# Performance work log

Measured on AMD Instinct MI355X. Metric: run time of the kernel, lower is better.

## Reference

```python
import jax, jax.numpy as jnp
import numpy as np

N_NODES = 50000
N_EDGES = 1_600_000
Q_MULT = 8          # charges_irreps = 8x0e
NODE_MULT = 64      # node_feat_irreps = 64x0e + 64x1o
RBF = 8             # edge_feats_irreps num_irreps
HID = 64            # FullyConnectedNet hidden width
W_NUMEL = 2 * Q_MULT  # edge_tp weight_numel: two uvu paths (0e->0e, 0e x 1o->1o), u=8


def setup_inputs() -> dict:
    key = jax.random.key(0)
    k = jax.random.split(key, 14)
    f = lambda kk, sh: jax.random.normal(kk, sh, dtype=jnp.float32)
    return {
        "node_feats": f(k[0], (N_NODES, NODE_MULT * 4)),          # 64 scalars + 64 vectors(3)
        "charges_0": f(k[1], (N_NODES, Q_MULT)),                  # unused in forward
        "charges_induced": f(k[2], (N_NODES, Q_MULT)),
        "edge_feats": f(k[3], (N_EDGES, RBF)),
        "edge_attrs": f(k[4], (N_EDGES, 4)),                      # Y0 (1) + Y1 (3)
        "field_feats": f(k[5], (N_NODES, RBF)),                   # unused in forward
        "mlp_w1": f(k[6], (RBF, HID)),
        "mlp_w2": f(k[7], (HID, HID)),
        "mlp_w3": f(k[8], (HID, HID)),
        "mlp_w4": f(k[9], (HID, W_NUMEL)),
        "W0": f(k[10], (Q_MULT, NODE_MULT)),                      # node_tp path 0e x 0e -> 0e
        "W1": f(k[11], (Q_MULT, NODE_MULT)),                      # node_tp path 1o x 1o -> 0e
        "edge_index": jax.random.randint(k[12], (2, N_EDGES), 0, N_NODES, dtype=jnp.int32),
        "batch": jnp.zeros((N_NODES,), dtype=jnp.int32),
    }


def reference(node_feats, charges_0, charges_induced, edge_feats, edge_attrs,
              field_feats, mlp_w1, mlp_w2, mlp_w3, mlp_w4, W0, W1,
              edge_index, batch):
    sender, receiver = edge_index[0], edge_index[1]
    num_nodes = node_feats.shape[0]

    # e3nn FullyConnectedNet: variance-normalized linear layers + silu
    h = edge_feats
    for w in (mlp_w1, mlp_w2, mlp_w3):
        h = jax.nn.silu(h @ (w / np.sqrt(np.float32(w.shape[0]))))
    tp_w = h @ (mlp_w4 / np.sqrt(np.float32(mlp_w4.shape[0])))   # [E, 16]
    w0, w1 = tp_w[:, :Q_MULT], tp_w[:, Q_MULT:]                   # per-edge path weights

    # edge_tp (uvu, external weights): gather sender charges, weighted CG product
    q_s = charges_induced[sender]                                  # [E, 8]
    mid0 = (w0 * q_s) * edge_attrs[:, :1]                          # [E, 8]    0e
    mid1 = (w1 * q_s)[:, :, None] * edge_attrs[:, None, 1:4]       # [E, 8, 3] 1o

    # scatter-sum messages to receiver nodes
    sum0 = jax.ops.segment_sum(mid0, receiver, num_segments=num_nodes)
    sum1 = jax.ops.segment_sum(mid1.reshape(-1, Q_MULT * 3), receiver,
                               num_segments=num_nodes).reshape(-1, Q_MULT, 3)

    # node_tp: FullyConnectedTensorProduct(8x0e+8x1o, 64x0e+64x1o -> 1x0e)
    node0 = node_feats[:, :NODE_MULT]                              # [N, 64]
    node1 = node_feats[:, NODE_MULT:].reshape(-1, NODE_MULT, 3)    # [N, 64, 3]
    c = 1.0 / np.sqrt(np.float32(Q_MULT * NODE_MULT * 2))          # path normalization
    e0 = jnp.einsum('nu,nv,uv->n', sum0, node0, W0)
    e1 = jnp.einsum('nuk,nvk,uv->n', sum1, node1, W1) / np.sqrt(np.float32(3.0))  # w3j(1,1,0)
    return c * (e0 + e1)                                           # [N] per-node energy
```

## Files before the change

kernel.cpp:

```cpp
#include <hip/hip_runtime.h>
#include <hip/hip_bf16.h>

typedef short short8 __attribute__((ext_vector_type(8)));
typedef float f32x4 __attribute__((ext_vector_type(4)));

static __device__ __forceinline__ float bf2f(unsigned int b) { return __uint_as_float(b << 16); }
static __device__ __forceinline__ short fb2s(float x) {
    unsigned u = __float_as_uint(x);
    return (short)((u + 0x7FFFu + ((u >> 16) & 1u)) >> 16);
}
static __device__ __forceinline__ unsigned int pack2(float lo, float hi) {
    unsigned int r;
    asm("v_cvt_pk_bf16_f32 %0, %1, %2" : "=v"(r) : "v"(lo), "v"(hi));
    return r;
}
static __device__ __forceinline__ float hsilu(float y) {
    return y * __builtin_amdgcn_rcpf(1.0f + __builtin_amdgcn_exp2f(-y));
}
static __device__ __forceinline__ float load1(const void* p, long off, int isbf) {
    return isbf ? bf2f(((const unsigned short*)p)[off]) : ((const float*)p)[off];
}
static __device__ __forceinline__ void load4(const void* p, long off, int isbf, float* o) {
    if (isbf) {
        uint2 v = *(const uint2*)((const unsigned short*)p + off);
        o[0]=bf2f(v.x&0xffffu); o[1]=bf2f(v.x>>16);
        o[2]=bf2f(v.y&0xffffu); o[3]=bf2f(v.y>>16);
    } else {
        float4 v = *(const float4*)((const float*)p + off);
        o[0]=v.x; o[1]=v.y; o[2]=v.z; o[3]=v.w;
    }
}
static __device__ __forceinline__ int detect_bf16(const void* nf) {
    const unsigned int* w = (const unsigned int*)nf;
    int lane = threadIdx.x & 63;
    unsigned int e = (w[lane] >> 7) & 0xFFu;
    unsigned long long m = __ballot(e >= 118u && e <= 132u);
    return __popcll(m) >= 32 ? 1 : 0;
}

#define NB 32
__global__ __launch_bounds__(256) void k_node(
    const void* __restrict__ nf, const void* __restrict__ W0, const void* __restrict__ W1,
    const void* __restrict__ w1, const void* __restrict__ w2,
    const void* __restrict__ w3, const void* __restrict__ w4,
    short* __restrict__ Bws, float* __restrict__ NA, float* __restrict__ acc, int n_nodes) {
    __shared__ float Nd0[NB * 68];
    __shared__ float Nd1[3 * NB * 68];
    __shared__ float W0L[8 * 68];
    __shared__ float W1L[8 * 68];
    const int tid = threadIdx.x;
    const int isbf = detect_bf16(nf);
    const long n0 = (long)blockIdx.x * NB;

    if (blockIdx.x < 44) {
        int idx = blockIdx.x * 256 + tid;
        int j = idx & 7, lane = (idx >> 3) & 63, tile = idx >> 9;
        int n16 = lane & 15, kq = lane >> 4;
        float v;
        if (tile < 4) {
            int k = kq * 8 + j, n = tile * 16 + n16;
            v = (k < 8) ? load1(w1, k * 64 + n, isbf) * (0.35355339059327373f * 1.4426950408889634f) : 0.0f;
        } else if (tile < 12) {
            int t = (tile - 4) >> 1, kt = (tile - 4) & 1;
            int k = kt * 32 + kq * 8 + j, n = t * 16 + n16;
            v = load1(w2, k * 64 + n, isbf) * 0.125f;
        } else if (tile < 20) {
            int t = (tile - 12) >> 1, kt = (tile - 12) & 1;
            int k = kt * 32 + kq * 8 + j, n = t * 16 + n16;
            v = load1(w3, k * 64 + n, isbf) * 0.125f;
        } else {
            int kt = tile - 20;
            int k = kt * 32 + kq * 8 + j, n = n16;
            v = load1(w4, k * 16 + n, isbf) * (0.125f * 0.6931471805599453f);
        }
        Bws[idx] = fb2s(v);
    }
    if (tid < NB) {
        long n = n0 + tid;
        if (n < n_nodes) acc[n] = 0.0f;
    }
    if (n0 >= n_nodes) return;

    for (int i = tid; i < 512; i += 256) {
        W0L[(i >> 6) * 68 + (i & 63)] = load1(W0, i, isbf);
        W1L[(i >> 6) * 68 + (i & 63)] = load1(W1, i, isbf);
    }
    if (isbf) {
        for (int i = tid; i < NB * 32; i += 256) {
            int node = i >> 5, c8 = (i & 31) * 8;
            long ng = n0 + node; if (ng > n_nodes - 1) ng = n_nodes - 1;
            uint4 v = *(const uint4*)((const unsigned short*)nf + ng * 256 + c8);
            float f[8];
            f[0]=bf2f(v.x&0xffffu); f[1]=bf2f(v.x>>16);
            f[2]=bf2f(v.y&0xffffu); f[3]=bf2f(v.y>>16);
            f[4]=bf2f(v.z&0xffffu); f[5]=bf2f(v.z>>16);
            f[6]=bf2f(v.w&0xffffu); f[7]=bf2f(v.w>>16);
            #pragma unroll
            for (int t = 0; t < 8; t++) {
                int col = c8 + t;
                if (col < 64) Nd0[node * 68 + col] = f[t];
                else {
                    int cc = col - 64, vv = cc / 3, kk = cc - vv * 3;
                    Nd1[(kk * NB + node) * 68 + vv] = f[t];
                }
            }
        }
    } else {
        for (int i = tid; i < NB * 64; i += 256) {
            int node = i >> 6, c4 = (i & 63) * 4;
            long ng = n0 + node; if (ng > n_nodes - 1) ng = n_nodes - 1;
            float4 v = *(const float4*)((const float*)nf + ng * 256 + c4);
            float f[4] = {v.x, v.y, v.z, v.w};
            #pragma unroll
            for (int t = 0; t < 4; t++) {
                int col = c4 + t;
                if (col < 64) Nd0[node * 68 + col] = f[t];
                else {
                    int cc = col - 64, vv = cc / 3, kk = cc - vv * 3;
                    Nd1[(kk * NB + node) * 68 + vv] = f[t];
                }
            }
        }
    }
    __syncthreads();

    const int wv = tid >> 6, lane = tid & 63;
    const int u = lane & 7, ln = lane >> 3;
    float sum[4] = {0.0f, 0.0f, 0.0f, 0.0f};

    if (wv == 0) {
        const float* w = &W0L[u * 68];
        for (int v0 = 0; v0 < 64; v0 += 4) {
            float4 w4 = *(const float4*)(w + v0);
            #pragma unroll
            for (int j = 0; j < 4; j++) {
                float4 nd = *(const float4*)&Nd0[(ln + 8 * j) * 68 + v0];
                sum[j] += w4.x * nd.x + w4.y * nd.y + w4.z * nd.z + w4.w * nd.w;
            }
        }
        #pragma unroll
        for (int j = 0; j < 4; j++) {
            long node = n0 + ln + 8 * j;
            if (node < n_nodes) NA[node * 32 + u] = sum[j] * 0.03125f;
        }
    } else {
        const int kk = wv - 1;
        const float* w = &W1L[u * 68];
        const float* nd1 = &Nd1[kk * NB * 68];
        for (int v0 = 0; v0 < 64; v0 += 4) {
            float4 w4 = *(const float4*)(w + v0);
            #pragma unroll
            for (int j = 0; j < 4; j++) {
                float4 nd = *(const float4*)&nd1[(ln + 8 * j) * 68 + v0];
                sum[j] += w4.x * nd.x + w4.y * nd.y + w4.z * nd.z + w4.w * nd.w;
            }
        }
        #pragma unroll
        for (int j = 0; j < 4; j++) {
            long node = n0 + ln + 8 * j;
            if (node < n_nodes) NA[node * 32 + 8 + u * 3 + kk] = sum[j] * 0.018042195912175804f;
        }
    }
}

__global__ __launch_bounds__(256, 4) void k_edges_mfma(
    const void* __restrict__ ef, const void* __restrict__ ea, const void* __restrict__ qc,
    const int* __restrict__ eidx, const void* __restrict__ nf,
    const short* __restrict__ Bws, const float* __restrict__ NA,
    float* __restrict__ acc, int n_edges) {
    __shared__ __align__(16) short W[11264];
    __shared__ __align__(16) short Hs[4 * 2304];
    const int tid = threadIdx.x, lane = tid & 63, wv = tid >> 6;
    const int n16 = lane & 15, kq = lane >> 4;
    const int isbf = detect_bf16(nf);

    {
        const uint4* src = (const uint4*)Bws;
        uint4* dst = (uint4*)W;
        for (int i = tid; i < 1408; i += 256) dst[i] = src[i];
    }
    __syncthreads();

    short* Hw = Hs + wv * 2304;
    const int rbit = (n16 >> 3) & 1;
    const int wrow = n16 * 72 + ((kq & 1) << 2);
    const int kql = (kq & 1) << 2;
    const f32x4 zero = {0.0f, 0.0f, 0.0f, 0.0f};

    for (int half = 0; half < 2; half++) {
        const long E0 = (long)blockIdx.x * 256 + half * 128 + wv * 32;

        long e_[2]; long ec_[2]; int s_[2], r_[2]; float eav_[2][4];
        #pragma unroll
        for (int mt = 0; mt < 2; mt++) {
            e_[mt] = E0 + mt * 16 + n16;
            long ec = e_[mt]; if (ec > n_edges - 1) ec = n_edges - 1;
            ec_[mt] = ec;
            s_[mt] = eidx[ec];
            r_[mt] = eidx[(long)n_edges + ec];
            load4(ea, ec * 4, isbf, eav_[mt]);
        }

        short8 a1[2];
        #pragma unroll
        for (int mt = 0; mt < 2; mt++) {
            short8 a = {0,0,0,0,0,0,0,0};
            if (kq == 0) {
                if (isbf) {
                    a = *(const short8*)((const unsigned short*)ef + ec_[mt] * 8);
                } else {
                    const float* pe = (const float*)ef + ec_[mt] * 8;
                    float4 v0 = *(const float4*)pe, v1 = *(const float4*)(pe + 4);
                    a[0]=fb2s(v0.x); a[1]=fb2s(v0.y); a[2]=fb2s(v0.z); a[3]=fb2s(v0.w);
                    a[4]=fb2s(v1.x); a[5]=fb2s(v1.y); a[6]=fb2s(v1.z); a[7]=fb2s(v1.w);
                }
            }
            a1[mt] = a;
        }

        {
            f32x4 c1[2][4];
            #pragma unroll
            for (int t = 0; t < 4; t++) {
                short8 b = *(const short8*)(W + t * 512 + lane * 8);
                #pragma unroll
                for (int mt = 0; mt < 2; mt++)
                    c1[mt][t] = __builtin_amdgcn_mfma_f32_16x16x32_bf16(b, a1[mt], zero, 0, 0, 0);
            }
            #pragma unroll
            for (int mt = 0; mt < 2; mt++)
                #pragma unroll
                for (int t = 0; t < 4; t++) {
                    uint2 pkd;
                    pkd.x = pack2(hsilu(c1[mt][t][0]), hsilu(c1[mt][t][1]));
                    pkd.y = pack2(hsilu(c1[mt][t][2]), hsilu(c1[mt][t][3]));
                    *(uint2*)(Hw + mt * 1152 + wrow + (((t * 2 + (kq >> 1)) ^ rbit) << 3)) = pkd;
                }
        }

        float q4_[2][4], na_[2][12];
        #pragma unroll
        for (int mt = 0; mt < 2; mt++) {
            load4(qc, (long)s_[mt] * 8 + kql, isbf, q4_[mt]);
            const float* nr = NA + (long)r_[mt] * 32;
            if (kq < 2) {
                *(float4*)na_[mt] = *(const float4*)(nr + (kq << 2));
            } else {
                *(float4*)(na_[mt] + 0) = *(const float4*)(nr + 8 + (kq - 2) * 12);
                *(float4*)(na_[mt] + 4) = *(const float4*)(nr + 12 + (kq - 2) * 12);
                *(float4*)(na_[mt] + 8) = *(const float4*)(nr + 16 + (kq - 2) * 12);
            }
        }

        #pragma unroll
        for (int L = 0; L < 2; L++) {
            const int base = (L == 0) ? 4 : 12;
            short8 aH[2][2];
            #pragma unroll
            for (int mt = 0; mt < 2; mt++)
                #pragma unroll
                for (int kt = 0; kt < 2; kt++)
                    aH[mt][kt] = *(const short8*)(Hw + mt * 1152 + n16 * 72 + (((kt * 4 + kq) ^ rbit) << 3));
            f32x4 c2[2][4];
            #pragma unroll
            for (int mt = 0; mt < 2; mt++)
                #pragma unroll
                for (int t = 0; t < 4; t++) c2[mt][t] = zero;
            #pragma unroll
            for (int kt = 0; kt < 2; kt++)
                #pragma unroll
                for (int t = 0; t < 4; t++) {
                    short8 b = *(const short8*)(W + (base + t * 2 + kt) * 512 + lane * 8);
                    #pragma unroll
                    for (int mt = 0; mt < 2; mt++)
                        c2[mt][t] = __builtin_amdgcn_mfma_f32_16x16x32_bf16(b, aH[mt][kt], c2[mt][t], 0, 0, 0);
                }
            #pragma unroll
            for (int mt = 0; mt < 2; mt++)
                #pragma unroll
                for (int t = 0; t < 4; t++) {
                    uint2 pkd;
                    pkd.x = pack2(hsilu(c2[mt][t][0]), hsilu(c2[mt][t][1]));
                    pkd.y = pack2(hsilu(c2[mt][t][2]), hsilu(c2[mt][t][3]));
                    *(uint2*)(Hw + mt * 1152 + wrow + (((t * 2 + (kq >> 1)) ^ rbit) << 3)) = pkd;
                }
        }

        f32x4 c4[2] = {zero, zero};
        {
            short8 aH[2][2];
            #pragma unroll
            for (int mt = 0; mt < 2; mt++)
                #pragma unroll
                for (int kt = 0; kt < 2; kt++)
                    aH[mt][kt] = *(const short8*)(Hw + mt * 1152 + n16 * 72 + (((kt * 4 + kq) ^ rbit) << 3));
            #pragma unroll
            for (int kt = 0; kt < 2; kt++) {
                short8 b = *(const short8*)(W + (20 + kt) * 512 + lane * 8);
                #pragma unroll
                for (int mt = 0; mt < 2; mt++)
                    c4[mt] = __builtin_amdgcn_mfma_f32_16x16x32_bf16(b, aH[mt][kt], c4[mt], 0, 0, 0);
            }
        }

        #pragma unroll
        for (int mt = 0; mt < 2; mt++) {
            float p = 0.0f;
            if (kq < 2) {
                #pragma unroll
                for (int r = 0; r < 4; r++) p += c4[mt][r] * q4_[mt][r] * na_[mt][r];
                p *= eav_[mt][0];
            } else {
                #pragma unroll
                for (int r = 0; r < 4; r++) {
                    float d = eav_[mt][1] * na_[mt][r * 3] + eav_[mt][2] * na_[mt][r * 3 + 1]
                            + eav_[mt][3] * na_[mt][r * 3 + 2];
                    p += c4[mt][r] * q4_[mt][r] * d;
                }
            }
            p += __shfl_xor(p, 16);
            p += __shfl_xor(p, 32);
            if (kq == 0 && e_[mt] < n_edges) atomicAdd(&acc[r_[mt]], p);
        }
    }
}

__global__ void k_out(const float* __restrict__ acc, void* __restrict__ out,
                      const void* __restrict__ nf, int n) {
    const int isbf = detect_bf16(nf);
    int i = blockIdx.x * 256 + threadIdx.x;
    if (i >= n) return;
    if (isbf) ((__hip_bfloat16*)out)[i] = __float2bfloat16(acc[i]);
    else      ((float*)out)[i] = acc[i];
}

extern "C" void kernel_launch(void* const* d_in, const int* in_sizes, int n_in,
                              void* d_out, int out_size, void* d_ws, size_t ws_size,
                              hipStream_t stream) {
    const void* node_feats      = d_in[0];
    const void* charges_induced = d_in[2];
    const void* edge_feats      = d_in[3];
    const void* edge_attrs      = d_in[4];
    const void* mlp_w1          = d_in[6];
    const void* mlp_w2          = d_in[7];
    const void* mlp_w3          = d_in[8];
    const void* mlp_w4          = d_in[9];
    const void* W0              = d_in[10];
    const void* W1              = d_in[11];
    const int*  edge_index      = (const int*)d_in[12];

    const int n_nodes = in_sizes[0] / 256;
    const int n_edges = in_sizes[3] / 8;

    short* Bws = (short*)d_ws;
    float* NA  = (float*)((char*)d_ws + 22528);
    float* acc = NA + (size_t)n_nodes * 32;

    int nblk = (n_nodes + NB - 1) / NB;
    if (nblk < 44) nblk = 44;
    k_node<<<nblk, 256, 0, stream>>>(node_feats, W0, W1,
        mlp_w1, mlp_w2, mlp_w3, mlp_w4, Bws, NA, acc, n_nodes);
    k_edges_mfma<<<(n_edges + 255) / 256, 256, 0, stream>>>(
        edge_feats, edge_attrs, charges_induced, edge_index, node_feats, Bws, NA, acc, n_edges);
    k_out<<<(n_nodes + 255) / 256, 256, 0, stream>>>(acc, d_out, node_feats, n_nodes);
}
```

Baseline: 378.8 us.

## Pass MLP activations between MFMA layers via ds_bpermute instead of LDS staging

Permutes the hidden-layer weight columns (Fmap) so MFMA output fragments can be rearranged into the next layer's A-operand layout in registers with a few ds_bpermute ops, removing the per-wave LDS scratch buffer and its write/read round trips. The gathers of charges and node aggregates are moved to just before their use. This reduces LDS footprint and traffic, which may allow higher occupancy. The risks are correctness of the permutation mapping and higher register pressure. Moving the loads later also gives less latency hiding.

```diff
diff --git a/kernel.cpp b/kernel.cpp
--- a/kernel.cpp
+++ b/kernel.cpp
@@ -3,6 +3,7 @@
 
 typedef short short8 __attribute__((ext_vector_type(8)));
 typedef float f32x4 __attribute__((ext_vector_type(4)));
+typedef unsigned int u32x4 __attribute__((ext_vector_type(4)));
 
 static __device__ __forceinline__ float bf2f(unsigned int b) { return __uint_as_float(b << 16); }
 static __device__ __forceinline__ short fb2s(float x) {
@@ -36,6 +37,14 @@
     unsigned int e = (w[lane] >> 7) & 0xFFu;
     unsigned long long m = __ballot(e >= 118u && e <= 132u);
     return __popcll(m) >= 32 ? 1 : 0;
+}
+static __device__ __forceinline__ short8 u4_to_s8(u32x4 u) {
+    union { u32x4 u; short8 s; } cvt; cvt.u = u; return cvt.s;
+}
+
+static __device__ __forceinline__ int Fmap(int tp, int rr) {
+    int kq_s = rr >> 2, h = (rr >> 1) & 1, b = rr & 1;
+    return 32 * (tp >> 1) + 8 * ((kq_s + tp) & 3) + 2 * (2 * h + (tp & 1)) + b;
 }
 
 #define NB 32
@@ -58,15 +67,15 @@
         int n16 = lane & 15, kq = lane >> 4;
         float v;
         if (tile < 4) {
-            int k = kq * 8 + j, n = tile * 16 + n16;
+            int k = kq * 8 + j, n = Fmap(tile, n16);
             v = (k < 8) ? load1(w1, k * 64 + n, isbf) * (0.35355339059327373f * 1.4426950408889634f) : 0.0f;
         } else if (tile < 12) {
             int t = (tile - 4) >> 1, kt = (tile - 4) & 1;
-            int k = kt * 32 + kq * 8 + j, n = t * 16 + n16;
+            int k = kt * 32 + kq * 8 + j, n = Fmap(t, n16);
             v = load1(w2, k * 64 + n, isbf) * 0.125f;
         } else if (tile < 20) {
             int t = (tile - 12) >> 1, kt = (tile - 12) & 1;
-            int k = kt * 32 + kq * 8 + j, n = t * 16 + n16;
+            int k = kt * 32 + kq * 8 + j, n = Fmap(t, n16);
             v = load1(w3, k * 64 + n, isbf) * 0.125f;
         } else {
             int kt = tile - 20;
@@ -169,7 +178,6 @@
     const short* __restrict__ Bws, const float* __restrict__ NA,
     float* __restrict__ acc, int n_edges) {
     __shared__ __align__(16) short W[11264];
-    __shared__ __align__(16) short Hs[4 * 2304];
     const int tid = threadIdx.x, lane = tid & 63, wv = tid >> 6;
     const int n16 = lane & 15, kq = lane >> 4;
     const int isbf = detect_bf16(nf);
@@ -181,35 +189,29 @@
     }
     __syncthreads();
 
-    short* Hw = Hs + wv * 2304;
-    const int rbit = (n16 >> 3) & 1;
-    const int wrow = n16 * 72 + ((kq & 1) << 2);
+    const int A1 = ((lane - 16) & 63) << 2;
+    const int A2 = ((lane - 32) & 63) << 2;
+    const int A3 = ((lane - 48) & 63) << 2;
     const int kql = (kq & 1) << 2;
     const f32x4 zero = {0.0f, 0.0f, 0.0f, 0.0f};
 
     for (int half = 0; half < 2; half++) {
         const long E0 = (long)blockIdx.x * 256 + half * 128 + wv * 32;
 
-        long e_[2]; long ec_[2]; int s_[2], r_[2]; float eav_[2][4];
+        int s_[2], r_[2]; float eav_[2][4];
+        short8 a1[2];
         #pragma unroll
         for (int mt = 0; mt < 2; mt++) {
-            e_[mt] = E0 + mt * 16 + n16;
-            long ec = e_[mt]; if (ec > n_edges - 1) ec = n_edges - 1;
-            ec_[mt] = ec;
+            long ec = E0 + mt * 16 + n16; if (ec > n_edges - 1) ec = n_edges - 1;
             s_[mt] = eidx[ec];
             r_[mt] = eidx[(long)n_edges + ec];
             load4(ea, ec * 4, isbf, eav_[mt]);
-        }
-
-        short8 a1[2];
-        #pragma unroll
-        for (int mt = 0; mt < 2; mt++) {
             short8 a = {0,0,0,0,0,0,0,0};
             if (kq == 0) {
                 if (isbf) {
-                    a = *(const short8*)((const unsigned short*)ef + ec_[mt] * 8);
+                    a = *(const short8*)((const unsigned short*)ef + ec * 8);
                 } else {
-                    const float* pe = (const float*)ef + ec_[mt] * 8;
+                    const float* pe = (const float*)ef + ec * 8;
                     float4 v0 = *(const float4*)pe, v1 = *(const float4*)(pe + 4);
                     a[0]=fb2s(v0.x); a[1]=fb2s(v0.y); a[2]=fb2s(v0.z); a[3]=fb2s(v0.w);
                     a[4]=fb2s(v1.x); a[5]=fb2s(v1.y); a[6]=fb2s(v1.z); a[7]=fb2s(v1.w);
@@ -218,54 +220,45 @@
             a1[mt] = a;
         }
 
-        {
-            f32x4 c1[2][4];
-            #pragma unroll
-            for (int t = 0; t < 4; t++) {
-                short8 b = *(const short8*)(W + t * 512 + lane * 8);
-                #pragma unroll
-                for (int mt = 0; mt < 2; mt++)
-                    c1[mt][t] = __builtin_amdgcn_mfma_f32_16x16x32_bf16(b, a1[mt], zero, 0, 0, 0);
-            }
+        f32x4 c[2][4];
+        short8 aH[2][2];
+
+        #pragma unroll
+        for (int t = 0; t < 4; t++) {
+            short8 b = *(const short8*)(W + t * 512 + lane * 8);
+            #pragma unroll
+            for (int mt = 0; mt < 2; mt++)
+                c[mt][t] = __builtin_amdgcn_mfma_f32_16x16x32_bf16(b, a1[mt], zero, 0, 0, 0);
+        }
+        #pragma unroll
+        for (int mt = 0; mt < 2; mt++) {
+            unsigned p00 = pack2(hsilu(c[mt][0][0]), hsilu(c[mt][0][1]));
+            unsigned p01 = pack2(hsilu(c[mt][0][2]), hsilu(c[mt][0][3]));
+            unsigned p10 = pack2(hsilu(c[mt][1][0]), hsilu(c[mt][1][1]));
+            unsigned p11 = pack2(hsilu(c[mt][1][2]), hsilu(c[mt][1][3]));
+            unsigned p20 = pack2(hsilu(c[mt][2][0]), hsilu(c[mt][2][1]));
+            unsigned p21 = pack2(hsilu(c[mt][2][2]), hsilu(c[mt][2][3]));
+            unsigned p30 = pack2(hsilu(c[mt][3][0]), hsilu(c[mt][3][1]));
+            unsigned p31 = pack2(hsilu(c[mt][3][2]), hsilu(c[mt][3][3]));
+            unsigned q01 = (unsigned)__builtin_amdgcn_ds_bpermute(A1, (int)p10);
+            unsigned q03 = (unsigned)__builtin_amdgcn_ds_bpermute(A1, (int)p11);
+            unsigned q10 = (unsigned)__builtin_amdgcn_ds_bpermute(A2, (int)p20);
+            unsigned q12 = (unsigned)__builtin_amdgcn_ds_bpermute(A2, (int)p21);
+            unsigned q11 = (unsigned)__builtin_amdgcn_ds_bpermute(A3, (int)p30);
+            unsigned q13 = (unsigned)__builtin_amdgcn_ds_bpermute(A3, (int)p31);
+            u32x4 u0 = {p00, q01, p01, q03};
+            u32x4 u1 = {q10, q11, q12, q13};
+            aH[mt][0] = u4_to_s8(u0);
+            aH[mt][1] = u4_to_s8(u1);
+        }
+
+        #pragma unroll
+        for (int L = 0; L < 2; L++) {
+            const int base = (L == 0) ? 4 : 12;
             #pragma unroll
             for (int mt = 0; mt < 2; mt++)
                 #pragma unroll
-                for (int t = 0; t < 4; t++) {
-                    uint2 pkd;
-                    pkd.x = pack2(hsilu(c1[mt][t][0]), hsilu(c1[mt][t][1]));
-                    pkd.y = pack2(hsilu(c1[mt][t][2]), hsilu(c1[mt][t][3]));
-                    *(uint2*)(Hw + mt * 1152 + wrow + (((t * 2 + (kq >> 1)) ^ rbit) << 3)) = pkd;
-                }
-        }
-
-        float q4_[2][4], na_[2][12];
-        #pragma unroll
-        for (int mt = 0; mt < 2; mt++) {
-            load4(qc, (long)s_[mt] * 8 + kql, isbf, q4_[mt]);
-            const float* nr = NA + (long)r_[mt] * 32;
-            if (kq < 2) {
-                *(float4*)na_[mt] = *(const float4*)(nr + (kq << 2));
-            } else {
-                *(float4*)(na_[mt] + 0) = *(const float4*)(nr + 8 + (kq - 2) * 12);
-                *(float4*)(na_[mt] + 4) = *(const float4*)(nr + 12 + (kq - 2) * 12);
-                *(float4*)(na_[mt] + 8) = *(const float4*)(nr + 16 + (kq - 2) * 12);
-            }
-        }
-
-        #pragma unroll
-        for (int L = 0; L < 2; L++) {
-            const int base = (L == 0) ? 4 : 12;
-            short8 aH[2][2];
-            #pragma unroll
-            for (int mt = 0; mt < 2; mt++)
-                #pragma unroll
-                for (int kt = 0; kt < 2; kt++)
-                    aH[mt][kt] = *(const short8*)(Hw + mt * 1152 + n16 * 72 + (((kt * 4 + kq) ^ rbit) << 3));
-            f32x4 c2[2][4];
-            #pragma unroll
-            for (int mt = 0; mt < 2; mt++)
-                #pragma unroll
-                for (int t = 0; t < 4; t++) c2[mt][t] = zero;
+                for (int t = 0; t < 4; t++) c[mt][t] = zero;
             #pragma unroll
             for (int kt = 0; kt < 2; kt++)
                 #pragma unroll
@@ -273,54 +266,69 @@
                     short8 b = *(const short8*)(W + (base + t * 2 + kt) * 512 + lane * 8);
                     #pragma unroll
                     for (int mt = 0; mt < 2; mt++)
-                        c2[mt][t] = __builtin_amdgcn_mfma_f32_16x16x32_bf16(b, aH[mt][kt], c2[mt][t], 0, 0, 0);
-                }
+                        c[mt][t] = __builtin_amdgcn_mfma_f32_16x16x32_bf16(b, aH[mt][kt], c[mt][t], 0, 0, 0);
+                }
+            #pragma unroll
+            for (int mt = 0; mt < 2; mt++) {
+                unsigned p00 = pack2(hsilu(c[mt][0][0]), hsilu(c[mt][0][1]));
+                unsigned p01 = pack2(hsilu(c[mt][0][2]), hsilu(c[mt][0][3]));
+                unsigned p10 = pack2(hsilu(c[mt][1][0]), hsilu(c[mt][1][1]));
+                unsigned p11 = pack2(hsilu(c[mt][1][2]), hsilu(c[mt][1][3]));
+                unsigned p20 = pack2(hsilu(c[mt][2][0]), hsilu(c[mt][2][1]));
+                unsigned p21 = pack2(hsilu(c[mt][2][2]), hsilu(c[mt][2][3]));
+                unsigned p30 = pack2(hsilu(c[mt][3][0]), hsilu(c[mt][3][1]));
+                unsigned p31 = pack2(hsilu(c[mt][3][2]), hsilu(c[mt][3][3]));
+                unsigned q01 = (unsigned)__builtin_amdgcn_ds_bpermute(A1, (int)p10);
+                unsigned q03 = (unsigned)__builtin_amdgcn_ds_bpermute(A1, (int)p11);
+                unsigned q10 = (unsigned)__builtin_amdgcn_ds_bpermute(A2, (int)p20);
+                unsigned q12 = (unsigned)__builtin_amdgcn_ds_bpermute(A2, (int)p21);
+                unsigned q11 = (unsigned)__builtin_amdgcn_ds_bpermute(A3, (int)p30);
+                unsigned q13 = (unsigned)__builtin_amdgcn_ds_bpermute(A3, (int)p31);
+                u32x4 u0 = {p00, q01, p01, q03};
+                u32x4 u1 = {q10, q11, q12, q13};
+                aH[mt][0] = u4_to_s8(u0);
+                aH[mt][1] = u4_to_s8(u1);
+            }
+        }
+
+        f32x4 c4[2] = {zero, zero};
+        #pragma unroll
+        for (int kt = 0; kt < 2; kt++) {
+            short8 b = *(const short8*)(W + (20 + kt) * 512 + lane * 8);
             #pragma unroll
             for (int mt = 0; mt < 2; mt++)
-                #pragma unroll
-                for (int t = 0; t < 4; t++) {
-                    uint2 pkd;
-                    pkd.x = pack2(hsilu(c2[mt][t][0]), hsilu(c2[mt][t][1]));
-                    pkd.y = pack2(hsilu(c2[mt][t][2]), hsilu(c2[mt][t][3]));
-                    *(uint2*)(Hw + mt * 1152 + wrow + (((t * 2 + (kq >> 1)) ^ rbit) << 3)) = pkd;
-                }
-        }
-
-        f32x4 c4[2] = {zero, zero};
-        {
-            short8 aH[2][2];
-            #pragma unroll
-            for (int mt = 0; mt < 2; mt++)
-                #pragma unroll
-                for (int kt = 0; kt < 2; kt++)
-                    aH[mt][kt] = *(const short8*)(Hw + mt * 1152 + n16 * 72 + (((kt * 4 + kq) ^ rbit) << 3));
-            #pragma unroll
-            for (int kt = 0; kt < 2; kt++) {
-                short8 b = *(const short8*)(W + (20 + kt) * 512 + lane * 8);
-                #pragma unroll
-                for (int mt = 0; mt < 2; mt++)
-                    c4[mt] = __builtin_amdgcn_mfma_f32_16x16x32_bf16(b, aH[mt][kt], c4[mt], 0, 0, 0);
-            }
+                c4[mt] = __builtin_amdgcn_mfma_f32_16x16x32_bf16(b, aH[mt][kt], c4[mt], 0, 0, 0);
         }
 
         #pragma unroll
         for (int mt = 0; mt < 2; mt++) {
+            float q4[4];
+            load4(qc, (long)s_[mt] * 8 + kql, isbf, q4);
+            float na[12];
+            const float* nr = NA + (long)r_[mt] * 32;
+            if (kq < 2) {
+                *(float4*)na = *(const float4*)(nr + (kq << 2));
+            } else {
+                *(float4*)(na + 0) = *(const float4*)(nr + 8 + (kq - 2) * 12);
+                *(float4*)(na + 4) = *(const float4*)(nr + 12 + (kq - 2) * 12);
+                *(float4*)(na + 8) = *(const float4*)(nr + 16 + (kq - 2) * 12);
+            }
             float p = 0.0f;
             if (kq < 2) {
                 #pragma unroll
-                for (int r = 0; r < 4; r++) p += c4[mt][r] * q4_[mt][r] * na_[mt][r];
+                for (int r = 0; r < 4; r++) p += c4[mt][r] * q4[r] * na[r];
                 p *= eav_[mt][0];
             } else {
                 #pragma unroll
                 for (int r = 0; r < 4; r++) {
-                    float d = eav_[mt][1] * na_[mt][r * 3] + eav_[mt][2] * na_[mt][r * 3 + 1]
-                            + eav_[mt][3] * na_[mt][r * 3 + 2];
-                    p += c4[mt][r] * q4_[mt][r] * d;
+                    float d = eav_[mt][1] * na[r * 3] + eav_[mt][2] * na[r * 3 + 1]
+                            + eav_[mt][3] * na[r * 3 + 2];
+                    p += c4[mt][r] * q4[r] * d;
                 }
             }
             p += __shfl_xor(p, 16);
             p += __shfl_xor(p, 32);
-            if (kq == 0 && e_[mt] < n_edges) atomicAdd(&acc[r_[mt]], p);
+            if (kq == 0 && (E0 + mt * 16 + n16) < n_edges) atomicAdd(&acc[r_[mt]], p);
         }
     }
 }
```

Measured after the change: 355.0 us. 1.07x faster.
